# Kernel optimization log

Hardware: AMD Instinct MI355X
Metric: run time of the kernel (lower is better)

The kernel has to match this reference:

```python
import jax, jax.numpy as jnp
import numpy as np

EPS = 1e-7  # K.epsilon()
NUM_ROUTING = 3


def squash(v, axis=-1):
    sq = jnp.sum(jnp.square(v), axis=axis, keepdims=True)
    return sq / (1.0 + sq) * (v / jnp.sqrt(sq + EPS))


def setup_inputs() -> dict:
    key = jax.random.key(0)
    k1, k2 = jax.random.split(key)
    B, NI, DI = 256, 1152, 8   # batch, input_num_capsule, input_dim_vector
    NJ, DJ = 10, 16            # num_capsule, dim_vector
    u = jax.random.normal(k1, (B, NI, DI), dtype=jnp.float32)
    W = jax.random.normal(k2, (NJ, NI, DJ, DI), dtype=jnp.float32) * 0.1
    return {"u": u, "W": W}


def reference(u, W):
    # u_hat[b,j,i,d] = sum_k u[b,i,k] * W[j,i,d,k]  (replaces tile + batch_dot)
    u_hat = jnp.einsum('bik,jidk->bjid', u, W)
    B, NJ, NI, _ = u_hat.shape
    b_ij = jnp.zeros((B, NJ, NI), dtype=u_hat.dtype)
    v_j = None
    for _ in range(NUM_ROUTING):
        c_ij = jax.nn.softmax(b_ij, axis=1)            # softmax over output capsules (dim=1)
        s_j = jnp.einsum('bji,bjid->bjd', c_ij, u_hat)  # weighted sum over input capsules
        v_j = squash(s_j)                               # (B, NJ, DJ)
        b_ij = b_ij + jnp.einsum('bjd,bjid->bji', v_j, u_hat)  # agreement update
    return v_j
```

## Files before the change

### kernel.cpp

```cpp
#include <hip/hip_runtime.h>
#include <math.h>

#define BB   256
#define NI   1152
#define DI   8
#define NJ   10
#define DJ   16
#define NCHUNK 18
#define CHUNK  64
#define BG     32
#define NBG    8
#define GRID_MAIN (NJ * NCHUNK * NBG)
#define BG2   8
#define GRID_BSA (8 * NCHUNK * (32 / 8))
#define CTP2 68

typedef _Float16 half2_t __attribute__((ext_vector_type(2)));
typedef _Float16 half4_t __attribute__((ext_vector_type(4)));
typedef _Float16 half8_t __attribute__((ext_vector_type(8)));
typedef float    f32x4   __attribute__((ext_vector_type(4)));

template <int CTRL>
__device__ __forceinline__ float dpp_add(float x) {
    int xi = __float_as_int(x);
    int yi = __builtin_amdgcn_update_dpp(0, xi, CTRL, 0xF, 0xF, true);
    return x + __int_as_float(yi);
}

__device__ __forceinline__ float dot16(half8_t w, half8_t uu) {
    half2_t w0 = {w[0], w[1]}, w1 = {w[2], w[3]}, w2 = {w[4], w[5]}, w3 = {w[6], w[7]};
    half2_t a0 = {uu[0], uu[1]}, a1 = {uu[2], uu[3]}, a2 = {uu[4], uu[5]}, a3 = {uu[6], uu[7]};
    float acc = __builtin_amdgcn_fdot2(w0, a0, 0.f, false);
    acc = __builtin_amdgcn_fdot2(w1, a1, acc, false);
    acc = __builtin_amdgcn_fdot2(w2, a2, acc, false);
    acc = __builtin_amdgcn_fdot2(w3, a3, acc, false);
    return acc;
}

struct Ctx {
    int j, chunk, bg, i0, b0, tid, il, dq, lane, w, g, xcd, local;
};

__device__ __forceinline__ Ctx make_ctx(int bid, int tid) {
    Ctx c;
    c.xcd = bid & 7; c.local = bid >> 3;
    int gx = c.xcd * (GRID_MAIN / 8) + c.local;
    c.j = gx % NJ; int r = gx / NJ;
    c.chunk = r % NCHUNK; c.bg = r / NCHUNK;
    c.i0 = c.chunk * CHUNK; c.b0 = c.bg * BG;
    c.tid = tid; c.il = tid >> 2; c.dq = tid & 3;
    c.lane = tid & 63; c.w = tid >> 6; c.g = (c.lane >> 4) & 3;
    return c;
}

__device__ __forceinline__ void loadWf(const _Float16* __restrict__ W16, const Ctx& cx,
                                       half8_t* Wf) {
    int drow = cx.lane & 15, ksub = cx.lane >> 4;
#pragma unroll
    for (int qq = 0; qq < 4; ++qq) {
        int i = cx.i0 + cx.w * 16 + qq * 4 + ksub;
        Wf[qq] = *(const half8_t*)(W16 + (((size_t)cx.j * NI + i) * DJ + drow) * DI);
    }
}

__global__ __launch_bounds__(256) void k_cvt(const float* __restrict__ uf,
                                             const float* __restrict__ Wf,
                                             _Float16* __restrict__ u16,
                                             _Float16* __restrict__ W16) {
    const int nu4 = (BB * NI * DI) / 4;
    int base = (blockIdx.x * 256 + threadIdx.x) * 4;
    if (base < nu4) {
#pragma unroll
        for (int t = 0; t < 4; ++t) {
            float4 v = ((const float4*)uf)[base + t];
            half4_t h = {(_Float16)v.x, (_Float16)v.y, (_Float16)v.z, (_Float16)v.w};
            ((half4_t*)u16)[base + t] = h;
        }
    } else {
        int k = base - nu4;
#pragma unroll
        for (int t = 0; t < 4; ++t) {
            float4 v = ((const float4*)Wf)[k + t];
            half4_t h = {(_Float16)v.x, (_Float16)v.y, (_Float16)v.z, (_Float16)v.w};
            ((half4_t*)W16)[k + t] = h;
        }
    }
}

__global__ __launch_bounds__(256) void k_A0m(const _Float16* __restrict__ u16,
                                             const _Float16* __restrict__ W16,
                                             float* __restrict__ spart) {
    __shared__ __align__(16) float sres2[2 * 4 * 16 * 17];
    Ctx cx = make_ctx(blockIdx.x, threadIdx.x);
    half8_t Wf[4];
    loadWf(W16, cx, Wf);
    int l = cx.lane, w = cx.w;
    int drow = l & 15, ksub = l >> 4;

    half8_t au[2][4];
#pragma unroll
    for (int h = 0; h < 2; ++h) {
        int b = cx.b0 + h * 16 + drow;
#pragma unroll
        for (int qq = 0; qq < 4; ++qq) {
            int il = w * 16 + qq * 4 + ksub;
            au[h][qq] = *(const half8_t*)(u16 + ((size_t)b * NI + cx.i0 + il) * DI);
        }
    }
#pragma unroll
    for (int h = 0; h < 2; ++h) {
        f32x4 acc = {0.f, 0.f, 0.f, 0.f};
#pragma unroll
        for (int qq = 0; qq < 4; ++qq)
            acc = __builtin_amdgcn_mfma_f32_16x16x32_f16(au[h][qq], Wf[qq], acc, 0, 0, 0);
#pragma unroll
        for (int r = 0; r < 4; ++r)
            sres2[((h * 4 + w) * 16 + ksub * 4 + r) * 17 + drow] = acc[r];
    }
    __syncthreads();
#pragma unroll
    for (int p = 0; p < 2; ++p) {
        int idx = p * 256 + cx.tid;
        int d = idx & 15, brow = (idx >> 4) & 15, h = idx >> 8;
        float s = 0.f;
#pragma unroll
        for (int w2 = 0; w2 < 4; ++w2)
            s += sres2[((h * 4 + w2) * 16 + brow) * 17 + d];
        s *= 0.1f;
        spart[(((size_t)cx.chunk * BB + cx.b0 + h * 16 + brow) * NJ + cx.j) * DJ + d] = s;
    }
}

template <int ACCUM>
__global__ __launch_bounds__(256) void k_BSA(const _Float16* __restrict__ u16,
                                             const _Float16* __restrict__ W16,
                                             float* __restrict__ spart,
                                             _Float16* __restrict__ delta) {
    __shared__ __align__(16) float     vsm[BG2 * NJ * DJ];
    __shared__ __align__(16) _Float16  dtile[BG2 * NJ * CHUNK];
    __shared__ __align__(16) _Float16  ctile[NJ * BG2 * CTP2];
    __shared__ __align__(16) float     sres[NJ * 4 * 8 * 17];

    int xcd = blockIdx.x & 7, local = blockIdx.x >> 3;
    int chunk = local % NCHUNK;
    int bgl   = local / NCHUNK;
    int b0 = xcd * 32 + bgl * BG2;
    int i0 = chunk * CHUNK;
    int tid = threadIdx.x;
    int lane = tid & 63, w = tid >> 6;

#pragma unroll
    for (int p = 0; p < 2; ++p) {
        int slot = p * 256 + tid;
        if (slot < BG2 * NJ * 4) {
            int b8 = slot / 40, rem = slot - b8 * 40;
            int j = rem >> 2, dq2 = rem & 3;
            int b = b0 + b8;
            float4 s4 = {0.f, 0.f, 0.f, 0.f};
#pragma unroll
            for (int ch = 0; ch < NCHUNK; ++ch) {
                float4 t = *(const float4*)&spart[(((size_t)ch * BB + b) * NJ + j) * DJ + dq2 * 4];
                s4.x += t.x; s4.y += t.y; s4.z += t.z; s4.w += t.w;
            }
            float sq = s4.x * s4.x + s4.y * s4.y + s4.z * s4.z + s4.w * s4.w;
            sq = dpp_add<0x0B1>(sq);
            sq = dpp_add<0x04E>(sq);
            float scale = (sq / (1.f + sq)) / sqrtf(sq + 1e-7f);
            float4 vv; vv.x = s4.x * scale; vv.y = s4.y * scale;
            vv.z = s4.z * scale; vv.w = s4.w * scale;
            *(float4*)&vsm[(b8 * NJ + j) * DJ + dq2 * 4] = vv;
        }
    }
    __syncthreads();

    int il = tid >> 2, dq = tid & 3;
    half8_t pu[BG2];
#pragma unroll
    for (int b8 = 0; b8 < BG2; ++b8)
        pu[b8] = *(const half8_t*)(u16 + ((size_t)(b0 + b8) * NI + i0 + il) * DI);

    for (int j = 0; j < NJ; ++j) {
        half8_t Wh[4];
        const half8_t* wp = (const half8_t*)(W16 +
            (((size_t)j * NI + i0 + il) * DJ + dq * 4) * DI);
#pragma unroll
        for (int q = 0; q < 4; ++q) Wh[q] = wp[q];
        float pj[BG2];
#pragma unroll
        for (int b8 = 0; b8 < BG2; ++b8) {
            float4 vv = *(const float4*)&vsm[(b8 * NJ + j) * DJ + dq * 4];
            float p = vv.x * dot16(Wh[0], pu[b8]);
            p = fmaf(vv.y, dot16(Wh[1], pu[b8]), p);
            p = fmaf(vv.z, dot16(Wh[2], pu[b8]), p);
            p = fmaf(vv.w, dot16(Wh[3], pu[b8]), p);
            p = dpp_add<0x0B1>(p);
            p = dpp_add<0x04E>(p);
            pj[b8] = p;
        }
        if (dq == 0) {
#pragma unroll
            for (int b8 = 0; b8 < BG2; ++b8)
                dtile[(b8 * NJ + j) * CHUNK + il] = (_Float16)pj[b8];
        }
    }
    __syncthreads();

#pragma unroll
    for (int p = 0; p < 5; ++p) {
        int slot = p * 256 + tid;
        int i4 = slot & 15, j = (slot >> 4) % NJ, b8 = slot / (NJ * 16);
        _Float16* dst = delta + (((size_t)(b0 + b8) * NJ + j) * NI + i0) + i4 * 4;
        half4_t raw = *(const half4_t*)&dtile[(b8 * NJ + j) * CHUNK + i4 * 4];
        if (ACCUM) {
            half4_t old = *(const half4_t*)dst;
            half4_t nw;
#pragma unroll
            for (int t = 0; t < 4; ++t) nw[t] = (_Float16)((float)raw[t] + (float)old[t]);
            *(half4_t*)dst = nw;
            *(half4_t*)&dtile[(b8 * NJ + j) * CHUNK + i4 * 4] = nw;
        } else {
            *(half4_t*)dst = raw;
        }
    }
    __syncthreads();

#pragma unroll
    for (int p = 0; p < 2; ++p) {
        int pair = p * 256 + tid;
        int b8 = pair >> 6, i = pair & 63;
        float x[NJ]; float ssum = 0.f;
#pragma unroll
        for (int j = 0; j < NJ; ++j) {
            x[j] = __expf((float)dtile[(b8 * NJ + j) * CHUNK + i]);
            ssum += x[j];
        }
        float rs = 1.f / ssum;
#pragma unroll
        for (int j = 0; j < NJ; ++j)
            ctile[(j * BG2 + b8) * CTP2 + i] = (_Float16)(x[j] * rs);
    }
    __syncthreads();

    int drow = lane & 15, ksub = lane >> 4;
    bool brow_ok = drow < BG2;
    half8_t au0[4];
#pragma unroll
    for (int qq = 0; qq < 4; ++qq) {
        int ili = w * 16 + qq * 4 + ksub;
        au0[qq] = brow_ok
            ? *(const half8_t*)(u16 + ((size_t)(b0 + drow) * NI + i0 + ili) * DI)
            : (half8_t){0, 0, 0, 0, 0, 0, 0, 0};
    }
    for (int j = 0; j < NJ; ++j) {
        half8_t Wfj[4];
#pragma unroll
        for (int qq = 0; qq < 4; ++qq) {
            int i = i0 + w * 16 + qq * 4 + ksub;
            Wfj[qq] = *(const half8_t*)(W16 + (((size_t)j * NI + i) * DJ + drow) * DI);
        }
        f32x4 acc = {0.f, 0.f, 0.f, 0.f};
#pragma unroll
        for (int qq = 0; qq < 4; ++qq) {
            int ili = w * 16 + qq * 4 + ksub;
            _Float16 ch = brow_ok ? ctile[(j * BG2 + drow) * CTP2 + ili] : (_Float16)0.f;
            half8_t cc = {ch, ch, ch, ch, ch, ch, ch, ch};
            acc = __builtin_amdgcn_mfma_f32_16x16x32_f16(au0[qq] * cc, Wfj[qq], acc, 0, 0, 0);
        }
        if (ksub < 2) {
#pragma unroll
            for (int r = 0; r < 4; ++r)
                sres[((j * 4 + w) * 8 + ksub * 4 + r) * 17 + drow] = acc[r];
        }
    }
    __syncthreads();
#pragma unroll
    for (int p = 0; p < 5; ++p) {
        int idx = p * 256 + tid;
        int d = idx & 15, brow = (idx >> 4) & 7, j = idx >> 7;
        float s = 0.f;
#pragma unroll
        for (int w2 = 0; w2 < 4; ++w2)
            s += sres[((j * 4 + w2) * 8 + brow) * 17 + d];
        spart[(((size_t)chunk * BB + b0 + brow) * NJ + j) * DJ + d] = s;
    }
}

__global__ __launch_bounds__(256) void k_V(const float* __restrict__ spart,
                                           float* __restrict__ out) {
    int idx4 = blockIdx.x * 256 + threadIdx.x;
    float4 s4 = {0.f, 0.f, 0.f, 0.f};
#pragma unroll
    for (int ch = 0; ch < NCHUNK; ++ch) {
        float4 t = *(const float4*)&spart[(size_t)ch * (BB * NJ * DJ) + (size_t)idx4 * 4];
        s4.x += t.x; s4.y += t.y; s4.z += t.z; s4.w += t.w;
    }
    float sq = s4.x * s4.x + s4.y * s4.y + s4.z * s4.z + s4.w * s4.w;
    sq = dpp_add<0x0B1>(sq);
    sq = dpp_add<0x04E>(sq);
    float scale = (sq / (1.f + sq)) / sqrtf(sq + 1e-7f);
    float4 o; o.x = s4.x * scale; o.y = s4.y * scale;
    o.z = s4.z * scale; o.w = s4.w * scale;
    *(float4*)&out[(size_t)idx4 * 4] = o;
}

extern "C" void kernel_launch(void* const* d_in, const int* in_sizes, int n_in,
                              void* d_out, int out_size, void* d_ws, size_t ws_size,
                              hipStream_t stream) {
    const float* u = (const float*)d_in[0];
    const float* W = (const float*)d_in[1];
    float* out = (float*)d_out;

    float*     spart = (float*)d_ws;
    _Float16*  delta = (_Float16*)(spart + (size_t)NCHUNK * BB * NJ * DJ);
    _Float16*  u16   = delta + (size_t)BB * NJ * NI;
    _Float16*  W16   = u16 + (size_t)BB * NI * DI;

    dim3 blk(256);
    const int GRID_CVT = ((BB * NI * DI) / 4 + (NJ * NI * DJ * DI) / 4) / (256 * 4);

    k_cvt<<<GRID_CVT, blk, 0, stream>>>(u, W, u16, W16);
    k_A0m<<<GRID_MAIN, blk, 0, stream>>>(u16, W16, spart);
    k_BSA<0><<<GRID_BSA, blk, 0, stream>>>(u16, W16, spart, delta);
    k_BSA<1><<<GRID_BSA, blk, 0, stream>>>(u16, W16, spart, delta);
    k_V<<<40, blk, 0, stream>>>(spart, out);
}
```

Baseline: 76.79 us.

## Replace stored routing logits with accumulated squash vectors; prefetch W tiles

Because b_ij is linear in v, the second routing pass now adds the first-iteration v_j (kept in a small vbuf) to the current v_j and recomputes the logits directly. This removes the global fp16 delta buffer and its read-modify-write traffic. The change also hoists the u loads to the top of the kernel and double-buffers W loads across the j loops to overlap memory with compute. The cost is extra register pressure and a small race-free vbuf write done only by chunk 0.

After: 76.00 us. About the same (-1.0%).

```diff
diff --git a/kernel.cpp b/kernel.cpp
--- a/kernel.cpp
+++ b/kernel.cpp
@@ -131,11 +131,11 @@
     }
 }
 
-template <int ACCUM>
+template <int ITER>
 __global__ __launch_bounds__(256) void k_BSA(const _Float16* __restrict__ u16,
                                              const _Float16* __restrict__ W16,
                                              float* __restrict__ spart,
-                                             _Float16* __restrict__ delta) {
+                                             float* __restrict__ vbuf) {
     __shared__ __align__(16) float     vsm[BG2 * NJ * DJ];
     __shared__ __align__(16) _Float16  dtile[BG2 * NJ * CHUNK];
     __shared__ __align__(16) _Float16  ctile[NJ * BG2 * CTP2];
@@ -148,6 +148,22 @@
     int i0 = chunk * CHUNK;
     int tid = threadIdx.x;
     int lane = tid & 63, w = tid >> 6;
+    int il = tid >> 2, dq = tid & 3;
+    int drow = lane & 15, ksub = lane >> 4;
+    bool brow_ok = drow < BG2;
+
+    half8_t pu[BG2];
+#pragma unroll
+    for (int b8 = 0; b8 < BG2; ++b8)
+        pu[b8] = *(const half8_t*)(u16 + ((size_t)(b0 + b8) * NI + i0 + il) * DI);
+    half8_t au0[4];
+#pragma unroll
+    for (int qq = 0; qq < 4; ++qq) {
+        int ili = w * 16 + qq * 4 + ksub;
+        au0[qq] = brow_ok
+            ? *(const half8_t*)(u16 + ((size_t)(b0 + drow) * NI + i0 + ili) * DI)
+            : (half8_t){0, 0, 0, 0, 0, 0, 0, 0};
+    }
 
 #pragma unroll
     for (int p = 0; p < 2; ++p) {
@@ -168,31 +184,39 @@
             float scale = (sq / (1.f + sq)) / sqrtf(sq + 1e-7f);
             float4 vv; vv.x = s4.x * scale; vv.y = s4.y * scale;
             vv.z = s4.z * scale; vv.w = s4.w * scale;
+            size_t va = ((size_t)b * NJ + j) * DJ + dq2 * 4;
+            if (ITER == 0) {
+                if (chunk == 0) *(float4*)&vbuf[va] = vv;
+            } else {
+                float4 v0 = *(const float4*)&vbuf[va];
+                vv.x += v0.x; vv.y += v0.y; vv.z += v0.z; vv.w += v0.w;
+            }
             *(float4*)&vsm[(b8 * NJ + j) * DJ + dq2 * 4] = vv;
         }
     }
     __syncthreads();
 
-    int il = tid >> 2, dq = tid & 3;
-    half8_t pu[BG2];
-#pragma unroll
-    for (int b8 = 0; b8 < BG2; ++b8)
-        pu[b8] = *(const half8_t*)(u16 + ((size_t)(b0 + b8) * NI + i0 + il) * DI);
-
+    half8_t WhA[4], WhB[4];
+    {
+        const half8_t* wp = (const half8_t*)(W16 + (((size_t)0 * NI + i0 + il) * DJ + dq * 4) * DI);
+#pragma unroll
+        for (int q = 0; q < 4; ++q) WhA[q] = wp[q];
+    }
     for (int j = 0; j < NJ; ++j) {
-        half8_t Wh[4];
-        const half8_t* wp = (const half8_t*)(W16 +
-            (((size_t)j * NI + i0 + il) * DJ + dq * 4) * DI);
-#pragma unroll
-        for (int q = 0; q < 4; ++q) Wh[q] = wp[q];
+        if (j + 1 < NJ) {
+            const half8_t* wp = (const half8_t*)(W16 +
+                (((size_t)(j + 1) * NI + i0 + il) * DJ + dq * 4) * DI);
+#pragma unroll
+            for (int q = 0; q < 4; ++q) WhB[q] = wp[q];
+        }
         float pj[BG2];
 #pragma unroll
         for (int b8 = 0; b8 < BG2; ++b8) {
             float4 vv = *(const float4*)&vsm[(b8 * NJ + j) * DJ + dq * 4];
-            float p = vv.x * dot16(Wh[0], pu[b8]);
-            p = fmaf(vv.y, dot16(Wh[1], pu[b8]), p);
-            p = fmaf(vv.z, dot16(Wh[2], pu[b8]), p);
-            p = fmaf(vv.w, dot16(Wh[3], pu[b8]), p);
+            float p = vv.x * dot16(WhA[0], pu[b8]);
+            p = fmaf(vv.y, dot16(WhA[1], pu[b8]), p);
+            p = fmaf(vv.z, dot16(WhA[2], pu[b8]), p);
+            p = fmaf(vv.w, dot16(WhA[3], pu[b8]), p);
             p = dpp_add<0x0B1>(p);
             p = dpp_add<0x04E>(p);
             pj[b8] = p;
@@ -202,24 +226,9 @@
             for (int b8 = 0; b8 < BG2; ++b8)
                 dtile[(b8 * NJ + j) * CHUNK + il] = (_Float16)pj[b8];
         }
-    }
-    __syncthreads();
-
-#pragma unroll
-    for (int p = 0; p < 5; ++p) {
-        int slot = p * 256 + tid;
-        int i4 = slot & 15, j = (slot >> 4) % NJ, b8 = slot / (NJ * 16);
-        _Float16* dst = delta + (((size_t)(b0 + b8) * NJ + j) * NI + i0) + i4 * 4;
-        half4_t raw = *(const half4_t*)&dtile[(b8 * NJ + j) * CHUNK + i4 * 4];
-        if (ACCUM) {
-            half4_t old = *(const half4_t*)dst;
-            half4_t nw;
-#pragma unroll
-            for (int t = 0; t < 4; ++t) nw[t] = (_Float16)((float)raw[t] + (float)old[t]);
-            *(half4_t*)dst = nw;
-            *(half4_t*)&dtile[(b8 * NJ + j) * CHUNK + i4 * 4] = nw;
-        } else {
-            *(half4_t*)dst = raw;
+        if (j + 1 < NJ) {
+#pragma unroll
+            for (int q = 0; q < 4; ++q) WhA[q] = WhB[q];
         }
     }
     __syncthreads();
@@ -241,22 +250,19 @@
     }
     __syncthreads();
 
-    int drow = lane & 15, ksub = lane >> 4;
-    bool brow_ok = drow < BG2;
-    half8_t au0[4];
+    half8_t WfA[4], WfB[4];
 #pragma unroll
     for (int qq = 0; qq < 4; ++qq) {
-        int ili = w * 16 + qq * 4 + ksub;
-        au0[qq] = brow_ok
-            ? *(const half8_t*)(u16 + ((size_t)(b0 + drow) * NI + i0 + ili) * DI)
-            : (half8_t){0, 0, 0, 0, 0, 0, 0, 0};
+        int i = i0 + w * 16 + qq * 4 + ksub;
+        WfA[qq] = *(const half8_t*)(W16 + (((size_t)0 * NI + i) * DJ + drow) * DI);
     }
     for (int j = 0; j < NJ; ++j) {
-        half8_t Wfj[4];
-#pragma unroll
-        for (int qq = 0; qq < 4; ++qq) {
-            int i = i0 + w * 16 + qq * 4 + ksub;
-            Wfj[qq] = *(const half8_t*)(W16 + (((size_t)j * NI + i) * DJ + drow) * DI);
+        if (j + 1 < NJ) {
+#pragma unroll
+            for (int qq = 0; qq < 4; ++qq) {
+                int i = i0 + w * 16 + qq * 4 + ksub;
+                WfB[qq] = *(const half8_t*)(W16 + (((size_t)(j + 1) * NI + i) * DJ + drow) * DI);
+            }
         }
         f32x4 acc = {0.f, 0.f, 0.f, 0.f};
 #pragma unroll
@@ -264,24 +270,28 @@
             int ili = w * 16 + qq * 4 + ksub;
             _Float16 ch = brow_ok ? ctile[(j * BG2 + drow) * CTP2 + ili] : (_Float16)0.f;
             half8_t cc = {ch, ch, ch, ch, ch, ch, ch, ch};
-            acc = __builtin_amdgcn_mfma_f32_16x16x32_f16(au0[qq] * cc, Wfj[qq], acc, 0, 0, 0);
+            acc = __builtin_amdgcn_mfma_f32_16x16x32_f16(au0[qq] * cc, WfA[qq], acc, 0, 0, 0);
         }
         if (ksub < 2) {
 #pragma unroll
             for (int r = 0; r < 4; ++r)
                 sres[((j * 4 + w) * 8 + ksub * 4 + r) * 17 + drow] = acc[r];
         }
+        if (j + 1 < NJ) {
+#pragma unroll
+            for (int qq = 0; qq < 4; ++qq) WfA[qq] = WfB[qq];
+        }
     }
     __syncthreads();
 #pragma unroll
     for (int p = 0; p < 5; ++p) {
         int idx = p * 256 + tid;
-        int d = idx & 15, brow = (idx >> 4) & 7, j = idx >> 7;
+        int d = idx & 15, brow2 = (idx >> 4) & 7, j = idx >> 7;
         float s = 0.f;
 #pragma unroll
         for (int w2 = 0; w2 < 4; ++w2)
-            s += sres[((j * 4 + w2) * 8 + brow) * 17 + d];
-        spart[(((size_t)chunk * BB + b0 + brow) * NJ + j) * DJ + d] = s;
+            s += sres[((j * 4 + w2) * 8 + brow2) * 17 + d];
+        spart[(((size_t)chunk * BB + b0 + brow2) * NJ + j) * DJ + d] = s;
     }
 }
 
@@ -311,8 +321,8 @@
     float* out = (float*)d_out;
 
     float*     spart = (float*)d_ws;
-    _Float16*  delta = (_Float16*)(spart + (size_t)NCHUNK * BB * NJ * DJ);
-    _Float16*  u16   = delta + (size_t)BB * NJ * NI;
+    float*     vbuf  = spart + (size_t)NCHUNK * BB * NJ * DJ;
+    _Float16*  u16   = (_Float16*)(vbuf + (size_t)BB * NJ * DJ);
     _Float16*  W16   = u16 + (size_t)BB * NI * DI;
 
     dim3 blk(256);
@@ -320,7 +330,7 @@
 
     k_cvt<<<GRID_CVT, blk, 0, stream>>>(u, W, u16, W16);
     k_A0m<<<GRID_MAIN, blk, 0, stream>>>(u16, W16, spart);
-    k_BSA<0><<<GRID_BSA, blk, 0, stream>>>(u16, W16, spart, delta);
-    k_BSA<1><<<GRID_BSA, blk, 0, stream>>>(u16, W16, spart, delta);
+    k_BSA<0><<<GRID_BSA, blk, 0, stream>>>(u16, W16, spart, vbuf);
+    k_BSA<1><<<GRID_BSA, blk, 0, stream>>>(u16, W16, spart, vbuf);
     k_V<<<40, blk, 0, stream>>>(spart, out);
 }
```
